# Kernel optimization log

Hardware: AMD Instinct MI355X
Metric: run time of the kernel (lower is better)

The kernel has to match this reference:

```python
import jax, jax.numpy as jnp
import numpy as np

HALF = 6.0
MAXC = 63.0
M_EMA = 0.999

def _pooled_ema(feature, pre, fea):
    # feature: [b,c,64,64]; pre: [b,21,2] float coords; fea: [21,c] EMA state
    b, c, H, W = feature.shape
    x = pre[..., 0]
    y = pre[..., 1]
    # torch: clamp then .int() (truncation == floor for non-negative values)
    down = jnp.maximum(y - HALF, 0.0).astype(jnp.int32)   # [b,21]
    left = jnp.maximum(x - HALF, 0.0).astype(jnp.int32)
    upper = jnp.minimum(y + HALF, MAXC).astype(jnp.int32)
    right = jnp.minimum(x + HALF, MAXC).astype(jnp.int32)
    # divisor uses inclusive window size (s1*s2), even though the torch slice
    # feature[:, left:right, down:upper] is exclusive at right/upper (faithful quirk)
    s = ((upper - down + 1) * (right - left + 1)).astype(feature.dtype)  # [b,21]
    # integral image (padded) -> rectangle sum over [left,right) x [down,upper)
    P = jnp.pad(jnp.cumsum(jnp.cumsum(feature, axis=2), axis=3),
                ((0, 0), (0, 0), (1, 0), (1, 0)))  # [b,c,H+1,W+1]
    bi = jnp.arange(b)[:, None]  # [b,1] broadcasts with [b,21] indices
    rect = (P[bi, :, right, upper] - P[bi, :, left, upper]
            - P[bi, :, right, down] + P[bi, :, left, down])  # [b,21,c]
    f4 = rect / s[..., None]          # per-landmark average pool [b,21,c]
    fea_c = f4.mean(axis=0)           # average over batch -> [21,c]
    return M_EMA * fea_c + (1.0 - M_EMA) * fea


def setup_inputs() -> dict:
    key = jax.random.key(0)
    k1, k2, k3, k4 = jax.random.split(key, 4)
    b, c, H, W, L = 64, 256, 64, 64, 21
    f1 = jax.random.uniform(k1, (b, c, H, W), dtype=jnp.float32)
    f2 = jax.random.uniform(k2, (b, c, H, W), dtype=jnp.float32)
    pre1 = jax.random.uniform(k3, (b, L, 2), dtype=jnp.float32) * 63.0
    pre2 = jax.random.uniform(k4, (b, L, 2), dtype=jnp.float32) * 63.0
    fea1 = jnp.zeros((L, c), dtype=jnp.float32)
    fea2 = jnp.zeros((L, c), dtype=jnp.float32)
    return {"f1": f1, "f2": f2, "pre1": pre1, "pre2": pre2,
            "fea1": fea1, "fea2": fea2}


def reference(f1, f2, pre1, pre2, fea1, fea2):
    fea_c1 = _pooled_ema(f1, pre1, fea1)               # [21,c]
    log_p = jax.nn.log_softmax(fea_c1, axis=-1)
    fea_c2 = _pooled_ema(f2, pre2, fea2)               # [21,c]
    q = fea_c2 / fea_c2.sum(axis=-1, keepdims=True)
    # KLDivLoss(reduction='none'): q * (log q - log_p), zero where q == 0
    kl = jnp.where(q > 0, q * (jnp.log(jnp.where(q > 0, q, 1.0)) - log_p), 0.0)
    return kl.sum(axis=-1).mean()
```

## Files before the change

### kernel.cpp

```cpp
#include <hip/hip_runtime.h>

#define NL 21
#define NC 256
#define NB 64
#define PSTRIDE 68

__global__ __launch_bounds__(256) void pool_kernel(
    const float* __restrict__ f1, const float* __restrict__ f2,
    const float* __restrict__ pre1, const float* __restrict__ pre2,
    float* __restrict__ part1, float* __restrict__ part2) {
    const int blk = blockIdx.x;
    const int b = blk >> 8;
    const int c = blk & 255;
    const float* __restrict__ feat = blockIdx.y ? f2 : f1;
    const float* __restrict__ pre  = blockIdx.y ? pre2 : pre1;
    float* __restrict__ outp       = blockIdx.y ? part2 : part1;

    __shared__ float plane[64 * PSTRIDE];
    __shared__ float part[256];
    __shared__ int s_left[NL], s_right[NL], s_down[NL], s_upper[NL];
    __shared__ float s_invs[NL];

    const int t = threadIdx.x;

    if (t < NL) {
        const float x = pre[(b * NL + t) * 2 + 0];
        const float y = pre[(b * NL + t) * 2 + 1];
        const int down  = (int)fmaxf(y - 6.0f, 0.0f);
        const int left  = (int)fmaxf(x - 6.0f, 0.0f);
        const int upper = (int)fminf(y + 6.0f, 63.0f);
        const int right = (int)fminf(x + 6.0f, 63.0f);
        s_left[t] = left; s_right[t] = right; s_down[t] = down; s_upper[t] = upper;
        s_invs[t] = 1.0f / (float)((upper - down + 1) * (right - left + 1));
    }

    const float4* __restrict__ src =
        (const float4*)(feat + ((size_t)b * NC + c) * 4096);
#pragma unroll
    for (int k = 0; k < 4; ++k) {
        const int f = t + k * 256;
        const int row = f >> 4;
        const int col4 = f & 15;
        const float4 v = src[f];
        float* dst = &plane[row * PSTRIDE + col4 * 4];
        dst[0] = v.x; dst[1] = v.y; dst[2] = v.z; dst[3] = v.w;
    }
    __syncthreads();

    float val = 0.0f;
    if (t < NL * 12) {
        const int l = t / 12;
        const int k = t - l * 12;
        const int h = s_left[l] + k;
        if (h < s_right[l]) {
            const float* row = &plane[h * PSTRIDE];
            const int d = s_down[l], u = s_upper[l];
            float s = 0.0f;
            for (int w = d; w < u; ++w) s += row[w];
            val = s;
        }
    }
    part[t] = val;
    __syncthreads();

    if (t < NL) {
        float r = 0.0f;
#pragma unroll
        for (int k = 0; k < 12; ++k) r += part[t * 12 + k];
        outp[((size_t)b * NL + t) * NC + c] = r * s_invs[t];
    }
}

__device__ __forceinline__ float wave_sum(float v) {
#pragma unroll
    for (int o = 32; o > 0; o >>= 1) v += __shfl_xor(v, o, 64);
    return v;
}
__device__ __forceinline__ float wave_max(float v) {
#pragma unroll
    for (int o = 32; o > 0; o >>= 1) v = fmaxf(v, __shfl_xor(v, o, 64));
    return v;
}
__device__ __forceinline__ float block_sum(float v, float* red) {
    v = wave_sum(v);
    const int wave = threadIdx.x >> 6, lane = threadIdx.x & 63;
    __syncthreads();
    if (lane == 0) red[wave] = v;
    __syncthreads();
    return red[0] + red[1] + red[2] + red[3];
}
__device__ __forceinline__ float block_max(float v, float* red) {
    v = wave_max(v);
    const int wave = threadIdx.x >> 6, lane = threadIdx.x & 63;
    __syncthreads();
    if (lane == 0) red[wave] = v;
    __syncthreads();
    return fmaxf(fmaxf(red[0], red[1]), fmaxf(red[2], red[3]));
}

__global__ __launch_bounds__(256) void finish_kernel(
    const float* __restrict__ part1, const float* __restrict__ part2,
    const float* __restrict__ fea1, const float* __restrict__ fea2,
    float* __restrict__ out) {
    const int c = threadIdx.x;
    __shared__ float red[4];
    __shared__ float sc1[NL][NC];
    __shared__ float sc2[NL][NC];

    float a1[NL], a2[NL];
#pragma unroll
    for (int l = 0; l < NL; ++l) { a1[l] = 0.0f; a2[l] = 0.0f; }
    for (int b = 0; b < NB; ++b) {
#pragma unroll
        for (int l = 0; l < NL; ++l) {
            a1[l] += part1[((size_t)b * NL + l) * NC + c];
            a2[l] += part2[((size_t)b * NL + l) * NC + c];
        }
    }
#pragma unroll
    for (int l = 0; l < NL; ++l) {
        sc1[l][c] = 0.999f * (a1[l] * (1.0f / 64.0f)) + 0.001f * fea1[l * NC + c];
        sc2[l][c] = 0.999f * (a2[l] * (1.0f / 64.0f)) + 0.001f * fea2[l * NC + c];
    }
    __syncthreads();

    double total = 0.0;
    for (int l = 0; l < NL; ++l) {
        const float x1 = sc1[l][c];
        const float x2 = sc2[l][c];

        const float m = block_max(x1, red);
        const float e = __expf(x1 - m);
        const float se = block_sum(e, red);
        const float logZ = m + logf(se);
        const float logp = x1 - logZ;

        const float ssum = block_sum(x2, red);
        const float q = x2 / ssum;

        const float kl = (q > 0.0f) ? q * (logf(q) - logp) : 0.0f;
        total += (double)block_sum(kl, red);
    }
    if (c == 0) out[0] = (float)(total / 21.0);
}

extern "C" void kernel_launch(void* const* d_in, const int* in_sizes, int n_in,
                              void* d_out, int out_size, void* d_ws, size_t ws_size,
                              hipStream_t stream) {
    const float* f1   = (const float*)d_in[0];
    const float* f2   = (const float*)d_in[1];
    const float* pre1 = (const float*)d_in[2];
    const float* pre2 = (const float*)d_in[3];
    const float* fea1 = (const float*)d_in[4];
    const float* fea2 = (const float*)d_in[5];
    float* out = (float*)d_out;

    float* part1 = (float*)d_ws;
    float* part2 = part1 + (size_t)NB * NL * NC;

    pool_kernel<<<dim3(NB * NC, 2), 256, 0, stream>>>(f1, f2, pre1, pre2, part1, part2);
    finish_kernel<<<1, 256, 0, stream>>>(part1, part2, fea1, fea2, out);
}
```

Before: 588.1 us.

## Double-buffer planes per block and parallelize batch reduction and KL finish

```diff
diff --git a/kernel.cpp b/kernel.cpp
--- a/kernel.cpp
+++ b/kernel.cpp
@@ -4,20 +4,22 @@
 #define NC 256
 #define NB 64
 #define PSTRIDE 68
+#define PPB 16
 
 __global__ __launch_bounds__(256) void pool_kernel(
     const float* __restrict__ f1, const float* __restrict__ f2,
     const float* __restrict__ pre1, const float* __restrict__ pre2,
     float* __restrict__ part1, float* __restrict__ part2) {
-    const int blk = blockIdx.x;
-    const int b = blk >> 8;
-    const int c = blk & 255;
-    const float* __restrict__ feat = blockIdx.y ? f2 : f1;
-    const float* __restrict__ pre  = blockIdx.y ? pre2 : pre1;
-    float* __restrict__ outp       = blockIdx.y ? part2 : part1;
+    const int p0   = blockIdx.x * PPB;
+    const int feat = p0 >> 14;
+    const int b    = (p0 >> 8) & 63;
+    const int c0   = p0 & 255;
+    const float* __restrict__ base = (feat ? f2 : f1) + (size_t)(b * NC + c0) * 4096;
+    const float* __restrict__ pre  = feat ? pre2 : pre1;
+    float* __restrict__ outp       = (feat ? part2 : part1) + (size_t)b * NL * NC;
 
-    __shared__ float plane[64 * PSTRIDE];
-    __shared__ float part[256];
+    __shared__ float buf[2][64 * PSTRIDE];
+    __shared__ float fold[256];
     __shared__ int s_left[NL], s_right[NL], s_down[NL], s_upper[NL];
     __shared__ float s_invs[NL];
 
@@ -34,114 +36,116 @@
         s_invs[t] = 1.0f / (float)((upper - down + 1) * (right - left + 1));
     }
 
-    const float4* __restrict__ src =
-        (const float4*)(feat + ((size_t)b * NC + c) * 4096);
-#pragma unroll
-    for (int k = 0; k < 4; ++k) {
-        const int f = t + k * 256;
-        const int row = f >> 4;
-        const int col4 = f & 15;
-        const float4 v = src[f];
-        float* dst = &plane[row * PSTRIDE + col4 * 4];
-        dst[0] = v.x; dst[1] = v.y; dst[2] = v.z; dst[3] = v.w;
+    float4 v0, v1, v2, v3;
+    {
+        const float4* __restrict__ src = (const float4*)base;
+        v0 = src[t]; v1 = src[t + 256]; v2 = src[t + 512]; v3 = src[t + 768];
+    }
+    {
+        float* d = buf[0];
+        *(float4*)&d[((t        ) >> 4) * PSTRIDE + ((t        ) & 15) * 4] = v0;
+        *(float4*)&d[((t + 256) >> 4) * PSTRIDE + ((t + 256) & 15) * 4] = v1;
+        *(float4*)&d[((t + 512) >> 4) * PSTRIDE + ((t + 512) & 15) * 4] = v2;
+        *(float4*)&d[((t + 768) >> 4) * PSTRIDE + ((t + 768) & 15) * 4] = v3;
     }
     __syncthreads();
 
-    float val = 0.0f;
-    if (t < NL * 12) {
-        const int l = t / 12;
-        const int k = t - l * 12;
-        const int h = s_left[l] + k;
-        if (h < s_right[l]) {
-            const float* row = &plane[h * PSTRIDE];
-            const int d = s_down[l], u = s_upper[l];
-            float s = 0.0f;
-            for (int w = d; w < u; ++w) s += row[w];
-            val = s;
+    for (int i = 0; i < PPB; ++i) {
+        const int cur = i & 1;
+        if (i + 1 < PPB) {
+            const float4* __restrict__ src = (const float4*)(base + (size_t)(i + 1) * 4096);
+            v0 = src[t]; v1 = src[t + 256]; v2 = src[t + 512]; v3 = src[t + 768];
         }
-    }
-    part[t] = val;
-    __syncthreads();
-
-    if (t < NL) {
-        float r = 0.0f;
+        float val = 0.0f;
+        if (t < NL * 12) {
+            const int l = t / 12;
+            const int kk = t - l * 12;
+            const int h = s_left[l] + kk;
+            if (h < s_right[l]) {
+                const float* row = &buf[cur][h * PSTRIDE];
+                const int d = s_down[l], u = s_upper[l];
+                float s = 0.0f;
+                for (int w = d; w < u; ++w) s += row[w];
+                val = s;
+            }
+        }
+        fold[t] = val;
+        __syncthreads();
+        if (t < NL) {
+            float r = 0.0f;
 #pragma unroll
-        for (int k = 0; k < 12; ++k) r += part[t * 12 + k];
-        outp[((size_t)b * NL + t) * NC + c] = r * s_invs[t];
+            for (int kk = 0; kk < 12; ++kk) r += fold[t * 12 + kk];
+            outp[t * NC + (c0 + i)] = r * s_invs[t];
+        }
+        if (i + 1 < PPB) {
+            float* d = buf[1 - cur];
+            *(float4*)&d[((t        ) >> 4) * PSTRIDE + ((t        ) & 15) * 4] = v0;
+            *(float4*)&d[((t + 256) >> 4) * PSTRIDE + ((t + 256) & 15) * 4] = v1;
+            *(float4*)&d[((t + 512) >> 4) * PSTRIDE + ((t + 512) & 15) * 4] = v2;
+            *(float4*)&d[((t + 768) >> 4) * PSTRIDE + ((t + 768) & 15) * 4] = v3;
+        }
+        __syncthreads();
     }
 }
 
-__device__ __forceinline__ float wave_sum(float v) {
-#pragma unroll
-    for (int o = 32; o > 0; o >>= 1) v += __shfl_xor(v, o, 64);
-    return v;
-}
-__device__ __forceinline__ float wave_max(float v) {
-#pragma unroll
-    for (int o = 32; o > 0; o >>= 1) v = fmaxf(v, __shfl_xor(v, o, 64));
-    return v;
-}
-__device__ __forceinline__ float block_sum(float v, float* red) {
-    v = wave_sum(v);
-    const int wave = threadIdx.x >> 6, lane = threadIdx.x & 63;
-    __syncthreads();
-    if (lane == 0) red[wave] = v;
-    __syncthreads();
-    return red[0] + red[1] + red[2] + red[3];
-}
-__device__ __forceinline__ float block_max(float v, float* red) {
-    v = wave_max(v);
-    const int wave = threadIdx.x >> 6, lane = threadIdx.x & 63;
-    __syncthreads();
-    if (lane == 0) red[wave] = v;
-    __syncthreads();
-    return fmaxf(fmaxf(red[0], red[1]), fmaxf(red[2], red[3]));
+__global__ __launch_bounds__(256) void reduce_kernel(
+    const float* __restrict__ part1, const float* __restrict__ part2,
+    const float* __restrict__ fea1, const float* __restrict__ fea2,
+    float* __restrict__ sc ) {
+    const int f = blockIdx.x / NL;
+    const int l = blockIdx.x - f * NL;
+    const int c = threadIdx.x;
+    const float* __restrict__ part = f ? part2 : part1;
+    const float* __restrict__ fea  = f ? fea2 : fea1;
+    float s = 0.0f;
+    for (int b = 0; b < NB; ++b) s += part[((size_t)b * NL + l) * NC + c];
+    sc[(f * NL + l) * NC + c] = 0.999f * (s * (1.0f / 64.0f)) + 0.001f * fea[l * NC + c];
 }
 
-__global__ __launch_bounds__(256) void finish_kernel(
-    const float* __restrict__ part1, const float* __restrict__ part2,
-    const float* __restrict__ fea1, const float* __restrict__ fea2,
-    float* __restrict__ out) {
-    const int c = threadIdx.x;
-    __shared__ float red[4];
-    __shared__ float sc1[NL][NC];
-    __shared__ float sc2[NL][NC];
+__global__ __launch_bounds__(256) void finish_kernel(const float* __restrict__ sc,
+                                                     float* __restrict__ out) {
+    const int t = threadIdx.x;
+    const int wave = t >> 6, lane = t & 63;
+    __shared__ float rowkl[NL];
 
-    float a1[NL], a2[NL];
+    for (int l = wave; l < NL; l += 4) {
+        const float* __restrict__ r1 = &sc[l * NC];
+        const float* __restrict__ r2 = &sc[(NL + l) * NC];
+        float x1[4], x2[4];
 #pragma unroll
-    for (int l = 0; l < NL; ++l) { a1[l] = 0.0f; a2[l] = 0.0f; }
-    for (int b = 0; b < NB; ++b) {
+        for (int j = 0; j < 4; ++j) { x1[j] = r1[lane + 64 * j]; x2[j] = r2[lane + 64 * j]; }
+
+        float m  = fmaxf(fmaxf(x1[0], x1[1]), fmaxf(x1[2], x1[3]));
+        float s2 = x2[0] + x2[1] + x2[2] + x2[3];
 #pragma unroll
-        for (int l = 0; l < NL; ++l) {
-            a1[l] += part1[((size_t)b * NL + l) * NC + c];
-            a2[l] += part2[((size_t)b * NL + l) * NC + c];
+        for (int o = 32; o > 0; o >>= 1) {
+            m  = fmaxf(m, __shfl_xor(m, o, 64));
+            s2 += __shfl_xor(s2, o, 64);
         }
-    }
+        float es = 0.0f;
 #pragma unroll
-    for (int l = 0; l < NL; ++l) {
-        sc1[l][c] = 0.999f * (a1[l] * (1.0f / 64.0f)) + 0.001f * fea1[l * NC + c];
-        sc2[l][c] = 0.999f * (a2[l] * (1.0f / 64.0f)) + 0.001f * fea2[l * NC + c];
+        for (int j = 0; j < 4; ++j) es += __expf(x1[j] - m);
+#pragma unroll
+        for (int o = 32; o > 0; o >>= 1) es += __shfl_xor(es, o, 64);
+        const float logZ = m + logf(es);
+        const float inv_s2 = 1.0f / s2;
+
+        float kl = 0.0f;
+#pragma unroll
+        for (int j = 0; j < 4; ++j) {
+            const float q = x2[j] * inv_s2;
+            if (q > 0.0f) kl += q * (logf(q) - (x1[j] - logZ));
+        }
+#pragma unroll
+        for (int o = 32; o > 0; o >>= 1) kl += __shfl_xor(kl, o, 64);
+        if (lane == 0) rowkl[l] = kl;
     }
     __syncthreads();
-
-    double total = 0.0;
-    for (int l = 0; l < NL; ++l) {
-        const float x1 = sc1[l][c];
-        const float x2 = sc2[l][c];
-
-        const float m = block_max(x1, red);
-        const float e = __expf(x1 - m);
-        const float se = block_sum(e, red);
-        const float logZ = m + logf(se);
-        const float logp = x1 - logZ;
-
-        const float ssum = block_sum(x2, red);
-        const float q = x2 / ssum;
-
-        const float kl = (q > 0.0f) ? q * (logf(q) - logp) : 0.0f;
-        total += (double)block_sum(kl, red);
+    if (t == 0) {
+        float tot = 0.0f;
+        for (int l = 0; l < NL; ++l) tot += rowkl[l];
+        out[0] = tot / 21.0f;
     }
-    if (c == 0) out[0] = (float)(total / 21.0);
 }
 
 extern "C" void kernel_launch(void* const* d_in, const int* in_sizes, int n_in,
@@ -157,7 +161,9 @@
 
     float* part1 = (float*)d_ws;
     float* part2 = part1 + (size_t)NB * NL * NC;
+    float* sc    = part2 + (size_t)NB * NL * NC;
 
-    pool_kernel<<<dim3(NB * NC, 2), 256, 0, stream>>>(f1, f2, pre1, pre2, part1, part2);
-    finish_kernel<<<1, 256, 0, stream>>>(part1, part2, fea1, fea2, out);
+    pool_kernel<<<dim3(2 * NB * NC / PPB), 256, 0, stream>>>(f1, f2, pre1, pre2, part1, part2);
+    reduce_kernel<<<dim3(2 * NL), 256, 0, stream>>>(part1, part2, fea1, fea2, sc);
+    finish_kernel<<<1, 256, 0, stream>>>(sc, out);
 }
```

After: 525.9 us. -10.6%, faster.
